# Performance work log

Measured on AMD Instinct MI355X. Metric: run time of the kernel, lower is better.

The kernel has to match this reference:

```python
import jax, jax.numpy as jnp
import numpy as np

B, S, D, NH, NKV, HD, FF = 2, 2048, 2048, 16, 8, 128, 8192
EPS = 1e-6
ROPE_THETA = 10000.0


def rmsnorm(x, w):
    return x * jax.lax.rsqrt(jnp.mean(x * x, axis=-1, keepdims=True) + EPS) * w


def rotate_half(x):
    h = x.shape[-1] // 2
    return jnp.concatenate([-x[..., h:], x[..., :h]], axis=-1)


def setup_inputs() -> dict:
    key = jax.random.key(0)
    ks = jax.random.split(key, 32)
    sc = 0.02
    inp = {}
    inp['x'] = jax.random.normal(ks[0], (B, S, D), dtype=jnp.float32)
    pos = jnp.arange(S, dtype=jnp.float32)
    inv = 1.0 / (ROPE_THETA ** (jnp.arange(0, HD, 2, dtype=jnp.float32) / HD))
    fr = jnp.outer(pos, inv)
    emb = jnp.concatenate([fr, fr], axis=-1)  # [S, HD]
    inp['cos'] = jnp.broadcast_to(jnp.cos(emb)[None], (B, S, HD)).astype(jnp.float32)
    inp['sin'] = jnp.broadcast_to(jnp.sin(emb)[None], (B, S, HD)).astype(jnp.float32)
    inp['vision_token_mask'] = jax.random.randint(ks[1], (B, S), 0, 2) > 0
    inp['attn_norm_w'] = jnp.ones((D,), jnp.float32)
    inp['ffn_norm_w'] = jnp.ones((D,), jnp.float32)
    shapes = {
        'wq': (D, NH * HD), 'wk': (D, NKV * HD), 'wv': (D, NKV * HD), 'wo': (NH * HD, D),
        'mm_wq': (D, NH * HD), 'mm_wk': (D, NKV * HD), 'mm_wv': (D, NKV * HD), 'mm_wo': (NH * HD, D),
        'gate_w': (D, FF), 'up_w': (D, FF), 'down_w': (FF, D),
        'mm_gate_w': (D, FF), 'mm_up_w': (D, FF), 'mm_down_w': (FF, D),
    }
    for i, (name, shp) in enumerate(shapes.items()):
        inp[name] = jax.random.normal(ks[2 + i], shp, dtype=jnp.float32) * sc
    for name in ['q_norm_w', 'k_norm_w', 'mm_q_norm_w', 'mm_k_norm_w']:
        inp[name] = jnp.ones((HD,), jnp.float32)
    return inp


def gpt_block(x, cos, sin, mask, attn_norm_w, ffn_norm_w,
              wq, wk, wv, wo, mm_wq, mm_wk, mm_wv, mm_wo,
              q_norm_w, k_norm_w, mm_q_norm_w, mm_k_norm_w,
              gate_w, up_w, down_w, mm_gate_w, mm_up_w, mm_down_w):
    m2 = mask[..., None]            # [B,S,1]
    m4 = mask[:, :, None, None]     # [B,S,1,1]
    h = rmsnorm(x, attn_norm_w)
    # dual-path QKV: text tokens use plain weights, vision tokens use mm_* weights
    q_t = rmsnorm((h @ wq).reshape(B, S, NH, HD), q_norm_w)
    q_v = rmsnorm((h @ mm_wq).reshape(B, S, NH, HD), mm_q_norm_w)
    q = jnp.where(m4, q_v, q_t)
    k_t = rmsnorm((h @ wk).reshape(B, S, NKV, HD), k_norm_w)
    k_v = rmsnorm((h @ mm_wk).reshape(B, S, NKV, HD), mm_k_norm_w)
    k = jnp.where(m4, k_v, k_t)
    v = jnp.where(m2, h @ mm_wv, h @ wv).reshape(B, S, NKV, HD)
    # RoPE (unsqueeze over head dim)
    cu = cos[:, :, None, :]
    su = sin[:, :, None, :]
    q = q * cu + rotate_half(q) * su
    k = k * cu + rotate_half(k) * su
    # GQA repeat + causal attention
    rep = NH // NKV
    k_r = jnp.repeat(k, rep, axis=2)
    v_r = jnp.repeat(v, rep, axis=2)
    scale = 1.0 / jnp.sqrt(jnp.float32(HD))
    scores = jnp.einsum('bqhd,bkhd->bhqk', q, k_r) * scale
    causal = jnp.tril(jnp.ones((S, S), bool))
    scores = jnp.where(causal, scores, jnp.float32(-1e30))
    p = jax.nn.softmax(scores, axis=-1)
    attn = jnp.einsum('bhqk,bkhd->bqhd', p, v_r).reshape(B, S, NH * HD)
    attn_out = jnp.where(m2, attn @ mm_wo, attn @ wo)
    h2 = x + attn_out
    # dual-path SwiGLU FFN
    g = rmsnorm(h2, ffn_norm_w)
    ff_t = (jax.nn.silu(g @ gate_w) * (g @ up_w)) @ down_w
    ff_v = (jax.nn.silu(g @ mm_gate_w) * (g @ mm_up_w)) @ mm_down_w
    return h2 + jnp.where(m2, ff_v, ff_t)


def reference(x, cos, sin, vision_token_mask, attn_norm_w, ffn_norm_w,
              wq, wk, wv, wo, mm_wq, mm_wk, mm_wv, mm_wo,
              q_norm_w, k_norm_w, mm_q_norm_w, mm_k_norm_w,
              gate_w, up_w, down_w, mm_gate_w, mm_up_w, mm_down_w):
    return gpt_block(x, cos, sin, vision_token_mask, attn_norm_w, ffn_norm_w,
                     wq, wk, wv, wo, mm_wq, mm_wk, mm_wv, mm_wo,
                     q_norm_w, k_norm_w, mm_q_norm_w, mm_k_norm_w,
                     gate_w, up_w, down_w, mm_gate_w, mm_up_w, mm_down_w)
```

## Files before the change

### kernel.cpp

```cpp
#include <hip/hip_runtime.h>

typedef unsigned short u16;
typedef __bf16 bf16x8 __attribute__((ext_vector_type(8)));
typedef float f32x4 __attribute__((ext_vector_type(4)));

__device__ __forceinline__ u16 f2bf(float f) {
    unsigned u = __builtin_bit_cast(unsigned, f);
    u += 0x7fffu + ((u >> 16) & 1u);
    return (u16)(u >> 16);
}
__device__ __forceinline__ float bf2f(u16 v) {
    unsigned u = ((unsigned)v) << 16;
    return __builtin_bit_cast(float, u);
}
__device__ __forceinline__ void glds16(const void* g, void* l) {
    __builtin_amdgcn_global_load_lds(
        (const __attribute__((address_space(1))) unsigned*)g,
        (__attribute__((address_space(3))) unsigned*)l, 16, 0, 0);
}

__device__ __forceinline__ void xcd_map(int bid, int nloc, int TM, int& tm, int& tn)
{
    const int xcd = bid & 7;
    int l = bid >> 3;
    const int per = nloc << 3;
    const int fullC = TM >> 3;
    const int lFull = fullC * per;
    int c, tn_l, tmIn;
    if (l < lFull) { c = l / per; int r = l - c * per; tn_l = r >> 3; tmIn = r & 7; }
    else { int r = l - lFull; int sc = TM - (fullC << 3); c = fullC; tn_l = r / sc; tmIn = r % sc; }
    tm = (c << 3) + tmIn;
    tn = xcd * nloc + tn_l;
}

__global__ __launch_bounds__(1024) void build_perm(
    const int* __restrict__ mask, int* __restrict__ perm, int* __restrict__ counts)
{
    __shared__ int sc[1024];
    int t = threadIdx.x;
    int m[4], cnt = 0;
#pragma unroll
    for (int j = 0; j < 4; j++) {
        m[j] = mask[t * 4 + j] != 0;
        cnt += (m[j] == 0);
    }
    sc[t] = cnt;
    __syncthreads();
    for (int off = 1; off < 1024; off <<= 1) {
        int v = (t >= off) ? sc[t - off] : 0;
        __syncthreads();
        sc[t] += v;
        __syncthreads();
    }
    int totT = sc[1023];
    int exT = sc[t] - cnt;
    int exV = t * 4 - exT;
    int pT = exT, pV = totT + exV;
#pragma unroll
    for (int j = 0; j < 4; j++) {
        if (m[j] == 0) perm[pT++] = t * 4 + j;
        else           perm[pV++] = t * 4 + j;
    }
    if (t == 0) { counts[0] = totT; counts[1] = 4096 - totT; }
}

__global__ __launch_bounds__(256) void transpose_bf16(
    const float* __restrict__ W, u16* __restrict__ Wt, int Kd, int Nd)
{
    __shared__ float tile[64][65];
    int k0 = blockIdx.x * 64, n0 = blockIdx.y * 64;
    int t = threadIdx.x;
    int rr = t >> 4, cc = (t & 15) * 4;
#pragma unroll
    for (int i = 0; i < 4; i++) {
        float4 v = *(const float4*)&W[(long)(k0 + i * 16 + rr) * Nd + n0 + cc];
        tile[i * 16 + rr][cc]     = v.x;
        tile[i * 16 + rr][cc + 1] = v.y;
        tile[i * 16 + rr][cc + 2] = v.z;
        tile[i * 16 + rr][cc + 3] = v.w;
    }
    __syncthreads();
    int nn = t >> 3, k8 = (t & 7) * 8;
#pragma unroll
    for (int i = 0; i < 2; i++) {
        int n = i * 32 + nn;
        u16 pk[8];
#pragma unroll
        for (int j = 0; j < 8; j++) pk[j] = f2bf(tile[k8 + j][n]);
        *(uint4*)&Wt[(long)(n0 + n) * Kd + k0 + k8] = *(const uint4*)pk;
    }
}

__global__ __launch_bounds__(256) void rms_x(
    const float* __restrict__ x, const float* __restrict__ w, u16* __restrict__ out)
{
    long row = blockIdx.x;
    int t = threadIdx.x, wave = t >> 6, lane = t & 63;
    const float4* x4 = (const float4*)(x + row * 2048);
    float4 a = x4[2 * t], b = x4[2 * t + 1];
    float ss = a.x*a.x + a.y*a.y + a.z*a.z + a.w*a.w
             + b.x*b.x + b.y*b.y + b.z*b.z + b.w*b.w;
#pragma unroll
    for (int m = 1; m < 64; m <<= 1) ss += __shfl_xor(ss, m);
    __shared__ float red[4];
    if (lane == 0) red[wave] = ss;
    __syncthreads();
    float tot = red[0] + red[1] + red[2] + red[3];
    float inv = rsqrtf(tot * (1.0f / 2048.0f) + 1e-6f);
    const float4* w4 = (const float4*)w;
    float4 wa = w4[2 * t], wb = w4[2 * t + 1];
    u16* op = out + row * 2048 + t * 8;
    op[0] = f2bf(a.x * inv * wa.x); op[1] = f2bf(a.y * inv * wa.y);
    op[2] = f2bf(a.z * inv * wa.z); op[3] = f2bf(a.w * inv * wa.w);
    op[4] = f2bf(b.x * inv * wb.x); op[5] = f2bf(b.y * inv * wb.y);
    op[6] = f2bf(b.z * inv * wb.z); op[7] = f2bf(b.w * inv * wb.w);
}

template <int EPI, bool PG, bool PC>
__global__ __launch_bounds__(512, 4) void gemm32(
    const u16* __restrict__ A, const u16* __restrict__ Bt0, const u16* __restrict__ Bt1,
    void* __restrict__ Cv,
    const int* __restrict__ perm, const int* __restrict__ counts, int N, int K)
{
    extern __shared__ u16 lds[];
    int tm, tn;
    xcd_map(blockIdx.x, N >> 11, 33, tm, tn);
    const int nT = counts[0];
    const int tT = (nT + 127) >> 7, tV = (4096 - nT + 127) >> 7;
    if (tm >= tT + tV) return;
    const bool vis = tm >= tT;
    const u16* Bt = vis ? Bt1 : Bt0;
    const int rowbase = vis ? nT + (tm - tT) * 128 : tm * 128;
    const int rowlim = vis ? 4096 : nT;
    const int tid = threadIdx.x;
    const int wave = tid >> 6, lane = tid & 63;
    const int wrbase = (wave >> 2) * 64, wcbase = (wave & 3) * 64;
    const int lr = lane & 15, lg = lane >> 4;
    const int n0 = tn * 256;
    const int t4 = tid >> 2, sp = tid & 3;
    const char* aSrc;
    const char* bSrc[2];
    {
        int r = t4;
        int gr = rowbase + r; gr = gr < 4095 ? gr : 4095;
        long ar = PG ? perm[gr] : gr;
        aSrc = (const char*)A + ar * (long)K * 2 + ((sp ^ (r & 3)) << 4);
    }
#pragma unroll
    for (int c = 0; c < 2; c++) {
        int r = c * 128 + t4;
        bSrc[c] = (const char*)Bt + (long)(n0 + r) * K * 2 + ((sp ^ (r & 3)) << 4);
    }
    auto stage = [&](int kt, int bu) {
        char* ab = (char*)lds + bu * 24576;
        long ko = (long)kt * 64;
        glds16(aSrc + ko, ab + tid * 16);
#pragma unroll
        for (int c = 0; c < 2; c++)
            glds16(bSrc[c] + ko, ab + 8192 + c * 8192 + tid * 16);
    };
    auto ldA = [&](int bu, int mi) -> bf16x8 {
        const char* ab = (const char*)lds + bu * 24576;
        int row = wrbase + mi * 16 + lr;
        return *(const bf16x8*)(ab + row * 64 + ((lg ^ (row & 3)) << 4));
    };
    auto ldB = [&](int bu, int ni) -> bf16x8 {
        const char* bb = (const char*)lds + bu * 24576 + 8192;
        int row = wcbase + ni * 16 + lr;
        return *(const bf16x8*)(bb + row * 64 + ((lg ^ (row & 3)) << 4));
    };

    f32x4 acc[4][4] = {};
    const int nkt = K >> 5;
    stage(0, 0);
    stage(1, 1);
    for (int kt = 0; kt < nkt; ++kt) {
        const int bu = kt % 3;
        if (kt == nkt - 1) asm volatile("s_waitcnt vmcnt(0)" ::: "memory");
        else               asm volatile("s_waitcnt vmcnt(3)" ::: "memory");
        __builtin_amdgcn_s_barrier();
        if (kt + 2 < nkt) stage(kt + 2, (kt + 2) % 3);
        bf16x8 af[4], bq[4];
#pragma unroll
        for (int i = 0; i < 4; i++) af[i] = ldA(bu, i);
#pragma unroll
        for (int j = 0; j < 4; j++) bq[j] = ldB(bu, j);
        __builtin_amdgcn_s_setprio(1);
#pragma unroll
        for (int i = 0; i < 4; i++)
#pragma unroll
            for (int j = 0; j < 4; j++)
                acc[i][j] = __builtin_amdgcn_mfma_f32_16x16x32_bf16(
                    af[i], bq[j], acc[i][j], 0, 0, 0);
        __builtin_amdgcn_s_setprio(0);
    }
#pragma unroll
    for (int mi = 0; mi < 4; mi++)
#pragma unroll
        for (int r = 0; r < 4; r++) {
            int gr = rowbase + wrbase + mi * 16 + lg * 4 + r;
            if (gr >= rowlim) continue;
            long crow = PC ? (long)perm[gr] : (long)gr;
#pragma unroll
            for (int ni = 0; ni < 4; ni++) {
                long col = n0 + wcbase + ni * 16 + lr;
                ((u16*)Cv)[crow * (long)N + col] = f2bf(acc[mi][ni][r]);
            }
        }
}

__global__ __launch_bounds__(512, 4) void gemm_gu(
    const u16* __restrict__ A,
    const u16* __restrict__ Bg0, const u16* __restrict__ Bg1,
    const u16* __restrict__ Bu0, const u16* __restrict__ Bu1,
    u16* __restrict__ C,
    const int* __restrict__ perm, const int* __restrict__ counts, int N, int K)
{
    extern __shared__ u16 lds[];
    int tm, tn;
    xcd_map(blockIdx.x, N >> 10, 33, tm, tn);
    const int nT = counts[0];
    const int tT = (nT + 127) >> 7, tV = (4096 - nT + 127) >> 7;
    if (tm >= tT + tV) return;
    const bool vis = tm >= tT;
    const u16* Bg = vis ? Bg1 : Bg0;
    const u16* Bu = vis ? Bu1 : Bu0;
    const int rowbase = vis ? nT + (tm - tT) * 128 : tm * 128;
    const int rowlim = vis ? 4096 : nT;
    const int tid = threadIdx.x;
    const int wave = tid >> 6, lane = tid & 63;
    const int wrbase = (wave >> 2) * 64, wcbase = (wave & 3) * 32;
    const int lr = lane & 15, lg = lane >> 4;
    const int n0 = tn * 128;
    const int t4 = tid >> 2, sp = tid & 3;
    const char *aSrc, *gSrc, *uSrc;
    {
        int r = t4;
        int gr = rowbase + r; gr = gr < 4095 ? gr : 4095;
        long ar = (long)perm[gr];
        aSrc = (const char*)A + ar * (long)K * 2 + ((sp ^ (r & 3)) << 4);
        gSrc = (const char*)Bg + (long)(n0 + r) * K * 2 + ((sp ^ (r & 3)) << 4);
        uSrc = (const char*)Bu + (long)(n0 + r) * K * 2 + ((sp ^ (r & 3)) << 4);
    }
    auto stage = [&](int kt, int bu) {
        char* ab = (char*)lds + bu * 24576;
        long ko = (long)kt * 64;
        glds16(aSrc + ko, ab + tid * 16);
        glds16(gSrc + ko, ab + 8192 + tid * 16);
        glds16(uSrc + ko, ab + 16384 + tid * 16);
    };
    auto ldA = [&](int bu, int mi) -> bf16x8 {
        const char* ab = (const char*)lds + bu * 24576;
        int row = wrbase + mi * 16 + lr;
        return *(const bf16x8*)(ab + row * 64 + ((lg ^ (row & 3)) << 4));
    };
    auto ldGU = [&](int bu, int sub, int ni) -> bf16x8 {
        const char* p = (const char*)lds + bu * 24576 + 8192 + sub * 8192;
        int row = wcbase + ni * 16 + lr;
        return *(const bf16x8*)(p + row * 64 + ((lg ^ (row & 3)) << 4));
    };

    f32x4 accg[4][2] = {}, accu[4][2] = {};
    const int nkt = K >> 5;
    stage(0, 0);
    stage(1, 1);
    for (int kt = 0; kt < nkt; ++kt) {
        const int bu = kt % 3;
        if (kt == nkt - 1) asm volatile("s_waitcnt vmcnt(0)" ::: "memory");
        else               asm volatile("s_waitcnt vmcnt(3)" ::: "memory");
        __builtin_amdgcn_s_barrier();
        if (kt + 2 < nkt) stage(kt + 2, (kt + 2) % 3);
        bf16x8 af[4], bg[2], bv[2];
#pragma unroll
        for (int i = 0; i < 4; i++) af[i] = ldA(bu, i);
#pragma unroll
        for (int j = 0; j < 2; j++) {
            bg[j] = ldGU(bu, 0, j);
            bv[j] = ldGU(bu, 1, j);
        }
        __builtin_amdgcn_s_setprio(1);
#pragma unroll
        for (int i = 0; i < 4; i++)
#pragma unroll
            for (int j = 0; j < 2; j++) {
                accg[i][j] = __builtin_amdgcn_mfma_f32_16x16x32_bf16(
                    af[i], bg[j], accg[i][j], 0, 0, 0);
                accu[i][j] = __builtin_amdgcn_mfma_f32_16x16x32_bf16(
                    af[i], bv[j], accu[i][j], 0, 0, 0);
            }
        __builtin_amdgcn_s_setprio(0);
    }
#pragma unroll
    for (int mi = 0; mi < 4; mi++)
#pragma unroll
        for (int r = 0; r < 4; r++) {
            int gr = rowbase + wrbase + mi * 16 + lg * 4 + r;
            if (gr >= rowlim) continue;
#pragma unroll
            for (int ni = 0; ni < 2; ni++) {
                long col = n0 + wcbase + ni * 16 + lr;
                float g = accg[mi][ni][r], u = accu[mi][ni][r];
                C[(long)gr * N + col] = f2bf(g / (1.0f + __expf(-g)) * u);
            }
        }
}

template <int EPI, bool PG, bool PC>
__global__ __launch_bounds__(512, 4) void gemmsq(
    const u16* __restrict__ A, const u16* __restrict__ Bt0, const u16* __restrict__ Bt1,
    void* __restrict__ Cv, const float* __restrict__ resid,
    const int* __restrict__ perm, const int* __restrict__ counts, int N, int K)
{
    extern __shared__ u16 lds[];
    int tm, tn;
    xcd_map(blockIdx.x, N >> 10, 33, tm, tn);
    const int nT = counts[0];
    const int tT = (nT + 127) >> 7, tV = (4096 - nT + 127) >> 7;
    if (tm >= tT + tV) return;
    const bool vis = tm >= tT;
    const u16* Bt = vis ? Bt1 : Bt0;
    const int rowbase = vis ? nT + (tm - tT) * 128 : tm * 128;
    const int rowlim = vis ? 4096 : nT;
    const int tid = threadIdx.x;
    const int wave = tid >> 6, lane = tid & 63;
    const int wrbase = (wave >> 2) * 64, wcbase = (wave & 3) * 32;
    const int lr = lane & 15, lg = lane >> 4;
    const int n0 = tn * 128;
    const int t4 = tid >> 2, sp = tid & 3;
    const char *aSrc, *bSrc;
    {
        int r = t4;
        int gr = rowbase + r; gr = gr < 4095 ? gr : 4095;
        long ar = PG ? (long)perm[gr] : (long)gr;
        aSrc = (const char*)A + ar * (long)K * 2 + ((sp ^ (r & 3)) << 4);
        bSrc = (const char*)Bt + (long)(n0 + r) * K * 2 + ((sp ^ (r & 3)) << 4);
    }
    auto stage = [&](int kt, int bu) {
        char* ab = (char*)lds + bu * 16384;
        long ko = (long)kt * 64;
        glds16(aSrc + ko, ab + tid * 16);
        glds16(bSrc + ko, ab + 8192 + tid * 16);
    };
    auto ldA = [&](int bu, int mi) -> bf16x8 {
        const char* ab = (const char*)lds + bu * 16384;
        int row = wrbase + mi * 16 + lr;
        return *(const bf16x8*)(ab + row * 64 + ((lg ^ (row & 3)) << 4));
    };
    auto ldB = [&](int bu, int ni) -> bf16x8 {
        const char* bb = (const char*)lds + bu * 16384 + 8192;
        int row = wcbase + ni * 16 + lr;
        return *(const bf16x8*)(bb + row * 64 + ((lg ^ (row & 3)) << 4));
    };

    f32x4 acc[4][2] = {};
    const int nkt = K >> 5;
    stage(0, 0);
    for (int kt = 0; kt < nkt; ++kt) {
        const int bu = kt & 1;
        __syncthreads();
        if (kt + 1 < nkt) stage(kt + 1, bu ^ 1);
        bf16x8 af[4], bq[2];
#pragma unroll
        for (int i = 0; i < 4; i++) af[i] = ldA(bu, i);
#pragma unroll
        for (int j = 0; j < 2; j++) bq[j] = ldB(bu, j);
        __builtin_amdgcn_s_setprio(1);
#pragma unroll
        for (int i = 0; i < 4; i++)
#pragma unroll
            for (int j = 0; j < 2; j++)
                acc[i][j] = __builtin_amdgcn_mfma_f32_16x16x32_bf16(
                    af[i], bq[j], acc[i][j], 0, 0, 0);
        __builtin_amdgcn_s_setprio(0);
    }
#pragma unroll
    for (int mi = 0; mi < 4; mi++)
#pragma unroll
        for (int r = 0; r < 4; r++) {
            int gr = rowbase + wrbase + mi * 16 + lg * 4 + r;
            if (gr >= rowlim) continue;
            long crow = PC ? (long)perm[gr] : (long)gr;
#pragma unroll
            for (int ni = 0; ni < 2; ni++) {
                long col = n0 + wcbase + ni * 16 + lr;
                long idx = crow * (long)N + col;
                ((float*)Cv)[idx] = resid[idx] + acc[mi][ni][r];
            }
        }
}

template <int EPI, bool PG, bool PC>
__global__ __launch_bounds__(512, 2) void gemmk(
    const u16* __restrict__ A, const u16* __restrict__ Bt0, const u16* __restrict__ Bt1,
    void* __restrict__ Cv, const float* __restrict__ resid,
    const int* __restrict__ perm, const int* __restrict__ counts, int N, int K)
{
    extern __shared__ u16 lds[];
    int tm, tn;
    xcd_map(blockIdx.x, N >> 11, 33, tm, tn);
    const int nT = counts[0];
    const int tT = (nT + 127) >> 7, tV = (4096 - nT + 127) >> 7;
    if (tm >= tT + tV) return;
    const bool vis = tm >= tT;
    const u16* Bt = vis ? Bt1 : Bt0;
    const int rowbase = vis ? nT + (tm - tT) * 128 : tm * 128;
    const int rowlim = vis ? 4096 : nT;
    const int tid = threadIdx.x;
    const int wave = tid >> 6, lane = tid & 63;
    const int wrbase = (wave >> 2) * 64, wcbase = (wave & 3) * 64;
    const int lr = lane & 15, lg = lane >> 4;
    const int n0 = tn * 256;
    const int t8 = tid >> 3, sp = tid & 7;
    const char* aSrc[2];
    const char* bSrc[4];
#pragma unroll
    for (int c = 0; c < 2; c++) {
        int r = c * 64 + t8;
        int gr = rowbase + r; gr = gr < 4095 ? gr : 4095;
        long ar = PG ? perm[gr] : gr;
        aSrc[c] = (const char*)A + ar * (long)K * 2 + ((sp ^ (r & 7)) << 4);
    }
#pragma unroll
    for (int c = 0; c < 4; c++) {
        int r = c * 64 + t8;
        bSrc[c] = (const char*)Bt + (long)(n0 + r) * K * 2 + ((sp ^ (r & 7)) << 4);
    }
    auto stage = [&](int kt, int bu) {
        char* ab = (char*)lds + bu * 49152;
        char* bb = ab + 16384;
        long ko = (long)kt * 128;
#pragma unroll
        for (int c = 0; c < 2; c++)
            glds16(aSrc[c] + ko, ab + c * 8192 + tid * 16);
#pragma unroll
        for (int c = 0; c < 4; c++)
            glds16(bSrc[c] + ko, bb + c * 8192 + tid * 16);
    };
    auto ldA = [&](int bu, int mi, int kk) -> bf16x8 {
        const char* ab = (const char*)lds + bu * 49152;
        int row = wrbase + mi * 16 + lr;
        int sl = kk * 4 + lg;
        return *(const bf16x8*)(ab + row * 128 + ((sl ^ (row & 7)) << 4));
    };
    auto ldB = [&](int bu, int ni, int kk) -> bf16x8 {
        const char* bb = (const char*)lds + bu * 49152 + 16384;
        int row = wcbase + ni * 16 + lr;
        int sl = kk * 4 + lg;
        return *(const bf16x8*)(bb + row * 128 + ((sl ^ (row & 7)) << 4));
    };

    f32x4 acc[4][4] = {};
    const int nkt = K >> 6;
    stage(0, 0);
    stage(1, 1);
    for (int kt = 0; kt < nkt; ++kt) {
        const int bu = kt % 3;
        if (kt == nkt - 1) asm volatile("s_waitcnt vmcnt(0)" ::: "memory");
        else               asm volatile("s_waitcnt vmcnt(6)" ::: "memory");
        __builtin_amdgcn_s_barrier();
        if (kt + 2 < nkt) stage(kt + 2, (kt + 2) % 3);
#pragma unroll
        for (int kk = 0; kk < 2; kk++) {
            bf16x8 af[4], bq[4];
#pragma unroll
            for (int i = 0; i < 4; i++) af[i] = ldA(bu, i, kk);
#pragma unroll
            for (int j = 0; j < 4; j++) bq[j] = ldB(bu, j, kk);
            __builtin_amdgcn_s_setprio(1);
#pragma unroll
            for (int i = 0; i < 4; i++)
#pragma unroll
                for (int j = 0; j < 4; j++)
                    acc[i][j] = __builtin_amdgcn_mfma_f32_16x16x32_bf16(
                        af[i], bq[j], acc[i][j], 0, 0, 0);
            __builtin_amdgcn_s_setprio(0);
        }
    }
#pragma unroll
    for (int mi = 0; mi < 4; mi++)
#pragma unroll
        for (int r = 0; r < 4; r++) {
            int gr = rowbase + wrbase + mi * 16 + lg * 4 + r;
            if (gr >= rowlim) continue;
            long crow = PC ? (long)perm[gr] : (long)gr;
#pragma unroll
            for (int ni = 0; ni < 4; ni++) {
                long col = n0 + wcbase + ni * 16 + lr;
                long idx = crow * (long)N + col;
                float v = acc[mi][ni][r];
                if (EPI == 1)      ((u16*)Cv)[idx] = f2bf(v);
                else if (EPI == 2) ((float*)Cv)[idx] = resid[idx] + v;
            }
        }
}

__global__ __launch_bounds__(256) void qk_fuse(
    const u16* __restrict__ p, const int* __restrict__ mask,
    const float* __restrict__ cs, const float* __restrict__ sn,
    const float* __restrict__ nwt, const float* __restrict__ nwv,
    u16* __restrict__ out, int H, int stride)
{
    int wave = threadIdx.x >> 6, lane = threadIdx.x & 63;
    int gw = blockIdx.x * 4 + wave;
    int tok = gw / H, h = gw % H;
    int b = tok >> 11, s = tok & 2047;
    const u16* src = p + (long)tok * stride + h * 128;
    const float* w = mask[tok] ? nwv : nwt;
    int d = lane * 2;
    float yx = bf2f(src[d]), yy = bf2f(src[d + 1]);
    float ss = yx * yx + yy * yy;
#pragma unroll
    for (int m = 1; m < 64; m <<= 1) ss += __shfl_xor(ss, m);
    float inv = rsqrtf(ss * (1.0f / 128.0f) + 1e-6f);
    float y0 = yx * inv * w[d], y1 = yy * inv * w[d + 1];
    float o0 = __shfl_xor(y0, 32), o1 = __shfl_xor(y1, 32);
    float sgn = (lane < 32) ? -1.0f : 1.0f;
    const float* cp = cs + (long)tok * 128 + d;
    const float* spn = sn + (long)tok * 128 + d;
    float r0 = y0 * cp[0] + sgn * o0 * spn[0];
    float r1 = y1 * cp[1] + sgn * o1 * spn[1];
    u16* op = out + (((long)b * H + h) * 2048 + s) * 128 + d;
    op[0] = f2bf(r0); op[1] = f2bf(r1);
}

__global__ __launch_bounds__(256) void v_fuse(
    const u16* __restrict__ vsrc, u16* __restrict__ outv, int stride)
{
    __shared__ u16 tile[32][33];
    int s0 = blockIdx.x * 32, d0 = blockIdx.y * 32;
    int bkv = blockIdx.z, b = bkv >> 3, kv = bkv & 7;
    int tx = threadIdx.x, ty = threadIdx.y;
#pragma unroll
    for (int i = 0; i < 32; i += 8) {
        long tok = (long)b * 2048 + s0 + ty + i;
        tile[ty + i][tx] = vsrc[tok * stride + kv * 128 + d0 + tx];
    }
    __syncthreads();
#pragma unroll
    for (int i = 0; i < 32; i += 8)
        outv[(((long)b * 8 + kv) * 128 + d0 + ty + i) * 2048 + s0 + tx] =
            tile[tx][ty + i];
}

__global__ __launch_bounds__(256) void attn_fwd(
    const u16* __restrict__ q, const u16* __restrict__ k,
    const u16* __restrict__ v, u16* __restrict__ out)
{
    __shared__ u16 Ks[32 * 128];
    __shared__ u16 Vs[128 * 32];
    __shared__ u16 Ps[4][16][40];
    const int tid = threadIdx.x, wave = tid >> 6, lane = tid & 63;
    const int lr = lane & 15, lg = lane >> 4;
    const int b = blockIdx.z, h = blockIdx.y, q0 = blockIdx.x * 64;
    const int kvh = h >> 1;
    const u16* qp = q + (((long)b * 16 + h) * 2048 + q0 + wave * 16) * 128;
    bf16x8 qf[4];
#pragma unroll
    for (int f = 0; f < 4; f++)
        qf[f] = *(const bf16x8*)(qp + (long)lr * 128 + f * 32 + lg * 8);
    const char* kbase = (const char*)(k + ((long)b * 8 + kvh) * 2048 * 128);
    const char* vbase = (const char*)(v + ((long)b * 8 + kvh) * 128 * 2048);
    f32x4 o[8] = {};
    float lsum[4] = {};
    const float sc2 = 0.08838834764831845f * 1.44269504088896f;
    const float MB = 16.5f;
    const int ntiles = (q0 + 64) >> 5;
    for (int t = 0; t < ntiles; ++t) {
        int kv0 = t * 32;
        __syncthreads();
#pragma unroll
        for (int j = 0; j < 2; j++) {
            int L = (j * 4 + wave) * 1024 + lane * 16;
            {
                int row = L >> 8, cb = L & 255;
                glds16(kbase + (long)(kv0 + row) * 256 + (cb ^ ((row & 7) << 4)),
                       (char*)Ks + (j * 4 + wave) * 1024);
            }
            {
                int row = L >> 6, cb = L & 63;
                glds16(vbase + (long)row * 4096 + kv0 * 2 + (cb ^ ((row & 3) << 4)),
                       (char*)Vs + (j * 4 + wave) * 1024);
            }
        }
        __syncthreads();
        f32x4 s[2] = {};
#pragma unroll
        for (int sub = 0; sub < 2; ++sub)
#pragma unroll
            for (int f = 0; f < 4; ++f) {
                int row = sub * 16 + lr;
                int cb = (f * 64 + lg * 16) ^ ((row & 7) << 4);
                bf16x8 kf = *(const bf16x8*)((const char*)Ks + row * 256 + cb);
                s[sub] = __builtin_amdgcn_mfma_f32_16x16x32_bf16(qf[f], kf, s[sub], 0, 0, 0);
            }
#pragma unroll
        for (int r = 0; r < 4; r++) {
            int rowg = q0 + wave * 16 + lg * 4 + r;
            float s0 = s[0][r] * sc2 - MB; if (kv0 + lr > rowg)      s0 = -1e30f;
            float s1 = s[1][r] * sc2 - MB; if (kv0 + 16 + lr > rowg) s1 = -1e30f;
            float p0 = exp2f(s0), p1 = exp2f(s1);
            lsum[r] += p0 + p1;
            int prow = lg * 4 + r;
            Ps[wave][prow][lr] = f2bf(p0);
            Ps[wave][prow][16 + lr] = f2bf(p1);
        }
        bf16x8 pf = *(const bf16x8*)&Ps[wave][lr][lg * 8];
#pragma unroll
        for (int ni = 0; ni < 8; ni++) {
            int row = ni * 16 + lr;
            int cb = (lg * 16) ^ ((row & 3) << 4);
            bf16x8 vf = *(const bf16x8*)((const char*)Vs + row * 64 + cb);
            o[ni] = __builtin_amdgcn_mfma_f32_16x16x32_bf16(pf, vf, o[ni], 0, 0, 0);
        }
    }
#pragma unroll
    for (int r = 0; r < 4; r++)
#pragma unroll
        for (int mm = 1; mm < 16; mm <<= 1) lsum[r] += __shfl_xor(lsum[r], mm);
#pragma unroll
    for (int ni = 0; ni < 8; ni++)
#pragma unroll
        for (int r = 0; r < 4; r++) {
            long row = (long)b * 2048 + q0 + wave * 16 + lg * 4 + r;
            out[row * 2048 + h * 128 + ni * 16 + lr] = f2bf(o[ni][r] / lsum[r]);
        }
}

extern "C" void kernel_launch(void* const* d_in, const int* in_sizes, int n_in,
                              void* d_out, int out_size, void* d_ws, size_t ws_size,
                              hipStream_t stream)
{
    const float* x    = (const float*)d_in[0];
    const float* cosp = (const float*)d_in[1];
    const float* sinp = (const float*)d_in[2];
    const int*   mask = (const int*)d_in[3];
    const float* anw  = (const float*)d_in[4];
    const float* fnw  = (const float*)d_in[5];
    const float* wq   = (const float*)d_in[6];
    const float* wk   = (const float*)d_in[7];
    const float* wv   = (const float*)d_in[8];
    const float* wo   = (const float*)d_in[9];
    const float* mwq  = (const float*)d_in[10];
    const float* mwk  = (const float*)d_in[11];
    const float* mwv  = (const float*)d_in[12];
    const float* mwo  = (const float*)d_in[13];
    const float* gw   = (const float*)d_in[14];
    const float* uw   = (const float*)d_in[15];
    const float* dw   = (const float*)d_in[16];
    const float* mgw  = (const float*)d_in[17];
    const float* muw  = (const float*)d_in[18];
    const float* mdw  = (const float*)d_in[19];
    const float* qnw  = (const float*)d_in[20];
    const float* knw  = (const float*)d_in[21];
    const float* mqnw = (const float*)d_in[22];
    const float* mknw = (const float*)d_in[23];

    char* base = (char*)d_ws;
    u16* wA0   = (u16*)(base);
    u16* wA1   = (u16*)(base + (32u << 20));
    u16* wB0   = (u16*)(base + (64u << 20));
    u16* wB1   = (u16*)(base + (96u << 20));
    u16* hbf   = (u16*)(base + (64u << 20));
    u16* qkv   = (u16*)(base + (80u << 20));
    u16* qb    = (u16*)(base + (112u << 20));
    u16* kb    = (u16*)(base + (128u << 20));
    u16* vb    = (u16*)(base + (136u << 20));
    u16* attnb = (u16*)(base + (144u << 20));
    u16* e1    = (u16*)(base + (128u << 20));
    float* h2  = (float*)(base + (192u << 20));
    u16* gbf   = (u16*)(base + (224u << 20));
    int* perm  = (int*)(base + (240u << 20));
    int* cnts  = perm + 4096;

    hipFuncSetAttribute((const void*)&gemm32<1, true, true>,
                        hipFuncAttributeMaxDynamicSharedMemorySize, 73728);
    hipFuncSetAttribute((const void*)&gemm_gu,
                        hipFuncAttributeMaxDynamicSharedMemorySize, 73728);
    hipFuncSetAttribute((const void*)&gemmk<2, true, true>,
                        hipFuncAttributeMaxDynamicSharedMemorySize, 147456);

    auto TR = [&](const float* w, u16* dst, int K, int N) {
        transpose_bf16<<<dim3(K / 64, N / 64), 256, 0, stream>>>(w, dst, K, N);
    };

    build_perm<<<1, 1024, 0, stream>>>(mask, perm, cnts);
    rms_x<<<4096, 256, 0, stream>>>(x, anw, hbf);

    TR(wq, wA0, 2048, 2048);
    TR(wk, wA0 + (long)2048 * 2048, 2048, 1024);
    TR(wv, wA0 + (long)3072 * 2048, 2048, 1024);
    TR(mwq, wA1, 2048, 2048);
    TR(mwk, wA1 + (long)2048 * 2048, 2048, 1024);
    TR(mwv, wA1 + (long)3072 * 2048, 2048, 1024);
    gemm32<1, true, true><<<528, 512, 73728, stream>>>(
        hbf, wA0, wA1, (void*)qkv, perm, cnts, 4096, 2048);

    qk_fuse<<<16384, 256, 0, stream>>>(qkv, mask, cosp, sinp, qnw, mqnw, qb, 16, 4096);
    qk_fuse<<<8192, 256, 0, stream>>>(qkv + 2048, mask, cosp, sinp, knw, mknw, kb, 8, 4096);
    v_fuse<<<dim3(64, 4, 16), dim3(32, 8), 0, stream>>>(qkv + 3072, vb, 4096);

    attn_fwd<<<dim3(32, 16, 2), 256, 0, stream>>>(qb, kb, vb, attnb);

    TR(wo, wA0, 2048, 2048); TR(mwo, wA1, 2048, 2048);
    gemmk<2, true, true><<<264, 512, 147456, stream>>>(
        attnb, wA0, wA1, (void*)h2, x, perm, cnts, 2048, 2048);

    rms_x<<<4096, 256, 0, stream>>>(h2, fnw, gbf);

    TR(gw, wA0, 2048, 8192); TR(mgw, wA1, 2048, 8192);
    TR(uw, wB0, 2048, 8192); TR(muw, wB1, 2048, 8192);
    gemm_gu<<<2112, 512, 73728, stream>>>(
        gbf, wA0, wA1, wB0, wB1, e1, perm, cnts, 8192, 2048);
    TR(dw, wA0, 8192, 2048); TR(mdw, wA1, 8192, 2048);
    gemmsq<2, false, true><<<528, 512, 32768, stream>>>(
        e1, wA0, wA1, (void*)d_out, h2, perm, cnts, 2048, 8192);
}
```

Measured before the change: 1.033 ms.

## Use 8-way XOR LDS swizzle in GEMMs and double-buffer gate/up GEMM

Replaces the 4-way XOR swizzle of the 64-byte LDS rows with an 8-way swizzle over row pairs (128-byte groups) in several GEMM kernels. Global-to-LDS source addresses are remapped so the direct LDS writes land in the swizzled positions. This is meant to reduce LDS bank conflicts on the fragment reads. Separately, gemm_gu drops from triple to double buffering, using less LDS and a higher occupancy hint so more blocks fit per CU, at the cost of a shallower prefetch pipeline.

```diff
diff --git a/kernel.cpp b/kernel.cpp
--- a/kernel.cpp
+++ b/kernel.cpp
@@ -31,6 +31,18 @@
     else { int r = l - lFull; int sc = TM - (fullC << 3); c = fullC; tn_l = r / sc; tmIn = r % sc; }
     tm = (c << 3) + tmIn;
     tn = xcd * nloc + tn_l;
+}
+
+__device__ __forceinline__ void swz_src(int r, int sp, int& rs, int& ks)
+{
+    int e = (((r & 1) << 2) | sp) ^ ((r >> 1) & 7);
+    rs = (r & ~1) | (e >> 2);
+    ks = e & 3;
+}
+__device__ __forceinline__ int swz_rd(int row, int lg)
+{
+    int s8 = (((row & 1) << 2) | lg) ^ ((row >> 1) & 7);
+    return (row >> 1) * 128 + s8 * 16;
 }
 
 __global__ __launch_bounds__(1024) void build_perm(
@@ -141,15 +153,16 @@
     const char* aSrc;
     const char* bSrc[2];
     {
-        int r = t4;
-        int gr = rowbase + r; gr = gr < 4095 ? gr : 4095;
+        int rs, ks; swz_src(t4, sp, rs, ks);
+        int gr = rowbase + rs; gr = gr < 4095 ? gr : 4095;
         long ar = PG ? perm[gr] : gr;
-        aSrc = (const char*)A + ar * (long)K * 2 + ((sp ^ (r & 3)) << 4);
+        aSrc = (const char*)A + ar * (long)K * 2 + ks * 16;
     }
 #pragma unroll
     for (int c = 0; c < 2; c++) {
         int r = c * 128 + t4;
-        bSrc[c] = (const char*)Bt + (long)(n0 + r) * K * 2 + ((sp ^ (r & 3)) << 4);
+        int rs, ks; swz_src(r, sp, rs, ks);
+        bSrc[c] = (const char*)Bt + (long)(n0 + rs) * K * 2 + ks * 16;
     }
     auto stage = [&](int kt, int bu) {
         char* ab = (char*)lds + bu * 24576;
@@ -162,12 +175,12 @@
     auto ldA = [&](int bu, int mi) -> bf16x8 {
         const char* ab = (const char*)lds + bu * 24576;
         int row = wrbase + mi * 16 + lr;
-        return *(const bf16x8*)(ab + row * 64 + ((lg ^ (row & 3)) << 4));
+        return *(const bf16x8*)(ab + swz_rd(row, lg));
     };
     auto ldB = [&](int bu, int ni) -> bf16x8 {
         const char* bb = (const char*)lds + bu * 24576 + 8192;
         int row = wcbase + ni * 16 + lr;
-        return *(const bf16x8*)(bb + row * 64 + ((lg ^ (row & 3)) << 4));
+        return *(const bf16x8*)(bb + swz_rd(row, lg));
     };
 
     f32x4 acc[4][4] = {};
@@ -209,7 +222,7 @@
         }
 }
 
-__global__ __launch_bounds__(512, 4) void gemm_gu(
+__global__ __launch_bounds__(512, 6) void gemm_gu(
     const u16* __restrict__ A,
     const u16* __restrict__ Bg0, const u16* __restrict__ Bg1,
     const u16* __restrict__ Bu0, const u16* __restrict__ Bu1,
@@ -235,12 +248,12 @@
     const int t4 = tid >> 2, sp = tid & 3;
     const char *aSrc, *gSrc, *uSrc;
     {
-        int r = t4;
-        int gr = rowbase + r; gr = gr < 4095 ? gr : 4095;
+        int rs, ks; swz_src(t4, sp, rs, ks);
+        int gr = rowbase + rs; gr = gr < 4095 ? gr : 4095;
         long ar = (long)perm[gr];
-        aSrc = (const char*)A + ar * (long)K * 2 + ((sp ^ (r & 3)) << 4);
-        gSrc = (const char*)Bg + (long)(n0 + r) * K * 2 + ((sp ^ (r & 3)) << 4);
-        uSrc = (const char*)Bu + (long)(n0 + r) * K * 2 + ((sp ^ (r & 3)) << 4);
+        aSrc = (const char*)A + ar * (long)K * 2 + ks * 16;
+        gSrc = (const char*)Bg + (long)(n0 + rs) * K * 2 + ks * 16;
+        uSrc = (const char*)Bu + (long)(n0 + rs) * K * 2 + ks * 16;
     }
     auto stage = [&](int kt, int bu) {
         char* ab = (char*)lds + bu * 24576;
@@ -252,24 +265,21 @@
     auto ldA = [&](int bu, int mi) -> bf16x8 {
         const char* ab = (const char*)lds + bu * 24576;
         int row = wrbase + mi * 16 + lr;
-        return *(const bf16x8*)(ab + row * 64 + ((lg ^ (row & 3)) << 4));
+        return *(const bf16x8*)(ab + swz_rd(row, lg));
     };
     auto ldGU = [&](int bu, int sub, int ni) -> bf16x8 {
         const char* p = (const char*)lds + bu * 24576 + 8192 + sub * 8192;
         int row = wcbase + ni * 16 + lr;
-        return *(const bf16x8*)(p + row * 64 + ((lg ^ (row & 3)) << 4));
+        return *(const bf16x8*)(p + swz_rd(row, lg));
     };
 
     f32x4 accg[4][2] = {}, accu[4][2] = {};
     const int nkt = K >> 5;
     stage(0, 0);
-    stage(1, 1);
     for (int kt = 0; kt < nkt; ++kt) {
-        const int bu = kt % 3;
-        if (kt == nkt - 1) asm volatile("s_waitcnt vmcnt(0)" ::: "memory");
-        else               asm volatile("s_waitcnt vmcnt(3)" ::: "memory");
-        __builtin_amdgcn_s_barrier();
-        if (kt + 2 < nkt) stage(kt + 2, (kt + 2) % 3);
+        const int bu = kt & 1;
+        __syncthreads();
+        if (kt + 1 < nkt) stage(kt + 1, bu ^ 1);
         bf16x8 af[4], bg[2], bv[2];
 #pragma unroll
         for (int i = 0; i < 4; i++) af[i] = ldA(bu, i);
@@ -329,11 +339,11 @@
     const int t4 = tid >> 2, sp = tid & 3;
     const char *aSrc, *bSrc;
     {
-        int r = t4;
-        int gr = rowbase + r; gr = gr < 4095 ? gr : 4095;
+        int rs, ks; swz_src(t4, sp, rs, ks);
+        int gr = rowbase + rs; gr = gr < 4095 ? gr : 4095;
         long ar = PG ? (long)perm[gr] : (long)gr;
-        aSrc = (const char*)A + ar * (long)K * 2 + ((sp ^ (r & 3)) << 4);
-        bSrc = (const char*)Bt + (long)(n0 + r) * K * 2 + ((sp ^ (r & 3)) << 4);
+        aSrc = (const char*)A + ar * (long)K * 2 + ks * 16;
+        bSrc = (const char*)Bt + (long)(n0 + rs) * K * 2 + ks * 16;
     }
     auto stage = [&](int kt, int bu) {
         char* ab = (char*)lds + bu * 16384;
@@ -344,12 +354,12 @@
     auto ldA = [&](int bu, int mi) -> bf16x8 {
         const char* ab = (const char*)lds + bu * 16384;
         int row = wrbase + mi * 16 + lr;
-        return *(const bf16x8*)(ab + row * 64 + ((lg ^ (row & 3)) << 4));
+        return *(const bf16x8*)(ab + swz_rd(row, lg));
     };
     auto ldB = [&](int bu, int ni) -> bf16x8 {
         const char* bb = (const char*)lds + bu * 16384 + 8192;
         int row = wcbase + ni * 16 + lr;
-        return *(const bf16x8*)(bb + row * 64 + ((lg ^ (row & 3)) << 4));
+        return *(const bf16x8*)(bb + swz_rd(row, lg));
     };
 
     f32x4 acc[4][2] = {};
@@ -675,7 +685,7 @@
     hipFuncSetAttribute((const void*)&gemm32<1, true, true>,
                         hipFuncAttributeMaxDynamicSharedMemorySize, 73728);
     hipFuncSetAttribute((const void*)&gemm_gu,
-                        hipFuncAttributeMaxDynamicSharedMemorySize, 73728);
+                        hipFuncAttributeMaxDynamicSharedMemorySize, 49152);
     hipFuncSetAttribute((const void*)&gemmk<2, true, true>,
                         hipFuncAttributeMaxDynamicSharedMemorySize, 147456);
 
@@ -709,7 +719,7 @@
 
     TR(gw, wA0, 2048, 8192); TR(mgw, wA1, 2048, 8192);
     TR(uw, wB0, 2048, 8192); TR(muw, wB1, 2048, 8192);
-    gemm_gu<<<2112, 512, 73728, stream>>>(
+    gemm_gu<<<2112, 512, 49152, stream>>>(
         gbf, wA0, wA1, wB0, wB1, e1, perm, cnts, 8192, 2048);
     TR(dw, wA0, 8192, 2048); TR(mdw, wA1, 8192, 2048);
     gemmsq<2, false, true><<<528, 512, 32768, stream>>>(
```

After: 3.412 ms. 230% more time.
